# Kernel optimization log

Measured on AMD Instinct MI355X. Metric: run time of the kernel, lower is better.

The kernel has to match this reference:

```python
import jax, jax.numpy as jnp
import numpy as np

N, M, D, O = 16384, 4096, 256, 256

def setup_inputs() -> dict:
    key = jax.random.key(0)
    k1, k2, k3, k4, k5, k6, k7 = jax.random.split(key, 7)
    H_fine = jax.random.normal(k1, (N, D), dtype=jnp.float32)
    H_coarse = jax.random.normal(k2, (M, D), dtype=jnp.float32)
    inter_channel_adj = jax.random.randint(k3, (N, M), 0, 2).astype(jnp.float32)
    # attention = nn.Linear(2D, 1): weight vector [2D], bias scalar
    wa = jax.random.normal(k4, (2 * D,), dtype=jnp.float32) * (1.0 / np.sqrt(2 * D))
    ba = jax.random.normal(k5, (1,), dtype=jnp.float32) * 0.01
    # transform = nn.Linear(D, O), xavier_uniform weight
    lim = np.sqrt(6.0 / (D + O)).astype(np.float32)
    Wt = jax.random.uniform(k6, (O, D), minval=-lim, maxval=lim, dtype=jnp.float32)
    bt = jax.random.normal(k7, (O,), dtype=jnp.float32) * 0.01
    return {"H_fine": H_fine, "H_coarse": H_coarse,
            "inter_channel_adj": inter_channel_adj,
            "wa": wa, "ba": ba, "Wt": Wt, "bt": bt}

def reference(H_fine, H_coarse, inter_channel_adj, wa, ba, Wt, bt):
    d = H_fine.shape[-1]
    # additive attention: score_ij = [hf_i ; hc_j] . wa + b
    # = hf_i . wa[:d] + hc_j . wa[d:] + b  (avoids [N,M,2D] concat)
    sf = H_fine @ wa[:d]            # [N]
    sc = H_coarse @ wa[d:]          # [M]
    scores = sf[:, None] + sc[None, :] + ba[0]        # [N, M]
    masked = scores * inter_channel_adj               # [N, M]
    weights = jax.nn.softmax(masked, axis=-1)         # [N, M]
    attn_out = weights @ H_coarse                     # [N, D]
    attn_out = attn_out + H_fine                      # add_self=True
    out = attn_out @ Wt.T + bt                        # [N, O]
    return jax.nn.relu(out)
```

## Files before the change

### kernel.cpp

```cpp
#include <hip/hip_runtime.h>
#include <hip/hip_fp16.h>
#include <stdint.h>

#define N_ 16384
#define M_ 4096
#define D_ 256
#define O_ 256

#define WS_T    0
#define WS_U    65536
#define WS_R    81920
#define WS_WTP  98304
#define WS_BP   229376

typedef float  f32x4  __attribute__((ext_vector_type(4)));
typedef _Float16 half8 __attribute__((ext_vector_type(8)));

__device__ __forceinline__ unsigned short f2h(float f) {
  __half h = __float2half(f);
  unsigned short u;
  __builtin_memcpy(&u, &h, 2);
  return u;
}
__device__ __forceinline__ uint32_t hpack(float a, float b) {
  __half2 h = __floats2half2_rn(a, b);
  uint32_t u;
  __builtin_memcpy(&u, &h, 4);
  return u;
}

__global__ __launch_bounds__(256) void prep_kernel(
    const float* __restrict__ Hf, const float* __restrict__ Hc,
    const float* __restrict__ wa, const float* __restrict__ ba,
    const float* __restrict__ Wt, float* __restrict__ tv,
    float* __restrict__ uv, unsigned short* __restrict__ BP,
    unsigned short* __restrict__ WtP, float* __restrict__ Rv) {
  __shared__ float tile[64][65];
  __shared__ float red[4][64];
  int b = blockIdx.x;
  int t = threadIdx.x;
  if (b < 5120) {
    int wv = t >> 6, lane = t & 63;
    const float* X; const float* w; const float* bias; float* outv; int row;
    if (b < 4096) { X = Hf; w = wa;      bias = ba;      outv = tv; row = b * 4 + wv; }
    else          { X = Hc; w = wa + D_; bias = nullptr; outv = uv; row = (b - 4096) * 4 + wv; }
    const float4* x4 = (const float4*)(X + (size_t)row * D_);
    const float4* w4 = (const float4*)w;
    float4 xa = x4[lane], wa4 = w4[lane];
    float s = xa.x * wa4.x + xa.y * wa4.y + xa.z * wa4.z + xa.w * wa4.w;
#pragma unroll
    for (int off = 32; off > 0; off >>= 1) s += __shfl_xor(s, off);
    if (lane == 0) outv[row] = expf(s + (bias ? bias[0] : 0.0f));
  } else if (b < 5376) {
    int bb = b - 5120;
    int bk = bb >> 2;
    int bc = bb & 3;
    int k0 = bk * 64, col0 = bc * 64;
    int lane = t & 63, wv = t >> 6;
    int m = lane & 15, q = lane >> 4;
    float colsum = 0.0f;
#pragma unroll
    for (int i = 0; i < 16; ++i) {
      int e = t + 256 * i;
      int kk = e >> 6, cc = e & 63;
      float v = Hc[(size_t)(k0 + kk) * D_ + col0 + cc];
      tile[kk][cc] = v;
      colsum += v;
    }
    red[wv][t & 63] = colsum;
    __syncthreads();
    if (t < 64)
      atomicAdd(&Rv[col0 + t], red[0][t] + red[1][t] + red[2][t] + red[3][t]);
#pragma unroll
    for (int t8 = 0; t8 < 2; ++t8) {
      int tile_id = t8 * 4 + wv;
      int sub = tile_id >> 2, g = tile_id & 3;
      int kgg = bk * 2 + sub;
      int cgg = bc * 4 + g;
      unsigned short v8[8];
#pragma unroll
      for (int j = 0; j < 8; ++j)
        v8[j] = f2h(tile[sub * 32 + q * 8 + j][g * 16 + m]);
      *(uint4*)(BP + ((size_t)(kgg * 16 + cgg) * 64 + lane) * 8) = *(uint4*)v8;
    }
  } else {
    int tt = (b - 5376) * 256 + t;
    int lane = tt & 63, cg = (tt >> 6) & 15, kg = tt >> 10;
    int m = lane & 15, q = lane >> 4;
    const float* src = Wt + (size_t)(cg * 16 + m) * D_ + kg * 32 + q * 8;
    float4 w0 = *(const float4*)src, w1 = *(const float4*)(src + 4);
    unsigned short v8[8];
    v8[0] = f2h(w0.x); v8[1] = f2h(w0.y); v8[2] = f2h(w0.z); v8[3] = f2h(w0.w);
    v8[4] = f2h(w1.x); v8[5] = f2h(w1.y); v8[6] = f2h(w1.z); v8[7] = f2h(w1.w);
    *(uint4*)(WtP + (size_t)tt * 8) = *(uint4*)v8;
  }
}

__device__ __forceinline__ half8 buildA(half8 a, __half2 th,
                                        const __half2* up, __half2 mone) {
  uint32_t ai[4], ro[4];
  __builtin_memcpy(ai, &a, 16);
#pragma unroll
  for (int k = 0; k < 4; ++k) {
    __half2 w2 = __hfma2(th, up[k], mone);
    __half2 av;
    __builtin_memcpy(&av, &ai[k], 4);
    __half2 r = __hmul2(av, w2);
    __builtin_memcpy(&ro[k], &r, 4);
  }
  half8 res;
  __builtin_memcpy(&res, ro, 16);
  return res;
}

#define LOADS(KB)                                                             \
  _Pragma("unroll")                                                           \
  for (int p = 0; p < 4; ++p)                                                 \
    na[p] = *(const float4*)(arow + (KB) + p * 64 + t15 * 4);

#define TAIL(BUF, KB)                                                         \
  _Pragma("unroll")                                                           \
  for (int p = 0; p < 4; ++p) {                                               \
    int col = (KB) + p * 64 + t15 * 4;                                        \
    float4 u4 = *(const float4*)&u_lds[col];                                  \
    su = fmaf(na[p].x, u4.x, su); su = fmaf(na[p].y, u4.y, su);               \
    su = fmaf(na[p].z, u4.z, su); su = fmaf(na[p].w, u4.w, su);               \
    sc += (na[p].x + na[p].y) + (na[p].z + na[p].w);                          \
    uint2 hv;                                                                 \
    hv.x = hpack(na[p].x, na[p].y);                                           \
    hv.y = hpack(na[p].z, na[p].w);                                           \
    *(uint2*)&A_lds[BUF][srow][p * 64 + t15 * 4] = hv;                        \
  }

#define COMPUTE(C, BUF)                                                       \
  _Pragma("unroll")                                                           \
  for (int kgl = 0; kgl < 8; ++kgl) {                                         \
    int kg = (C) * 8 + kgl;                                                   \
    const unsigned short* bp = BP + ((size_t)(kg * 16 + w * 2)) * 512 + (size_t)lane * 8; \
    half8 bf0 = *(const half8*)(bp);                                          \
    half8 bf1 = *(const half8*)(bp + 512);                                    \
    uint4 uu = *(const uint4*)&u_h2[kg * 16 + q * 4];                         \
    __half2 up[4];                                                            \
    __builtin_memcpy(up, &uu, 16);                                            \
    half8 a0 = *(const half8*)&A_lds[BUF][m][kgl * 32 + q * 8];               \
    half8 a1 = *(const half8*)&A_lds[BUF][16 + m][kgl * 32 + q * 8];          \
    half8 af0 = buildA(a0, th0, up, mone);                                    \
    half8 af1 = buildA(a1, th1, up, mone);                                    \
    acc[0][0] = __builtin_amdgcn_mfma_f32_16x16x32_f16(af0, bf0, acc[0][0], 0, 0, 0); \
    acc[0][1] = __builtin_amdgcn_mfma_f32_16x16x32_f16(af0, bf1, acc[0][1], 0, 0, 0); \
    acc[1][0] = __builtin_amdgcn_mfma_f32_16x16x32_f16(af1, bf0, acc[1][0], 0, 0, 0); \
    acc[1][1] = __builtin_amdgcn_mfma_f32_16x16x32_f16(af1, bf1, acc[1][1], 0, 0, 0); \
  }

__global__ __launch_bounds__(512, 4) void mega_kernel(
    const float* __restrict__ adj, const unsigned short* __restrict__ BP,
    const float* __restrict__ tv, const float* __restrict__ uv,
    const float* __restrict__ Rv, const float* __restrict__ Hf,
    const unsigned short* __restrict__ WtP, const float* __restrict__ bt,
    float* __restrict__ out) {
  __shared__ __align__(16) char smem[59520];
  unsigned short (*A_lds)[32][272] = (unsigned short (*)[32][272])(smem);
  float* u_lds = (float*)(smem + 34816);
  uint32_t* u_h2 = (uint32_t*)(smem + 51200);
  float* Lsum_lds = (float*)(smem + 59392);
  unsigned short (*attn)[264] = (unsigned short (*)[264])(smem);

  int tid = threadIdx.x;
  int w = tid >> 6, lane = tid & 63;
  int q = lane >> 4, m = lane & 15;
  int srow = tid >> 4, t15 = tid & 15;
  int i0 = blockIdx.x * 32;

  const float* arow = adj + ((size_t)i0 + srow) * M_;
  float su = 0.f, sc = 0.f;
  float4 na[4];

  LOADS(0)

  for (int i = tid; i < M_ / 2; i += 512) {
    float2 u2 = *(const float2*)(uv + 2 * i);
    u_lds[2 * i] = u2.x; u_lds[2 * i + 1] = u2.y;
    u_h2[i] = hpack(u2.x, u2.y);
  }

  __half2 th0 = __float2half2_rn(tv[i0 + m]);
  __half2 th1 = __float2half2_rn(tv[i0 + 16 + m]);
  const __half2 mone = __float2half2_rn(-1.0f);

  f32x4 acc[2][2];
#pragma unroll
  for (int s = 0; s < 2; ++s)
#pragma unroll
    for (int n = 0; n < 2; ++n) acc[s][n] = (f32x4){0.f, 0.f, 0.f, 0.f};

  __syncthreads();
  TAIL(0, 0)
  __syncthreads();

#pragma unroll 1
  for (int c = 0; c < 16; ++c) {
    if (c < 15) { LOADS((c + 1) * 256) }
    COMPUTE(c, c & 1)
    if (c < 15) { TAIL((c + 1) & 1, (c + 1) * 256) }
    __syncthreads();
  }

#pragma unroll
  for (int off = 1; off < 16; off <<= 1) {
    su += __shfl_xor(su, off);
    sc += __shfl_xor(sc, off);
  }
  if (t15 == 0)
    Lsum_lds[srow] = tv[i0 + srow] * su - sc;
  __syncthreads();

  {
    float rv0 = Rv[w * 32 + m];
    float rv1 = Rv[w * 32 + 16 + m];
#pragma unroll
    for (int rt = 0; rt < 2; ++rt)
#pragma unroll
      for (int r = 0; r < 4; ++r) {
        int row = rt * 16 + q * 4 + r;
        float invL = 1.0f / (Lsum_lds[row] + (float)M_);
        size_t grow = (size_t)i0 + row;
        float h0 = Hf[grow * D_ + w * 32 + m];
        float h1 = Hf[grow * D_ + w * 32 + 16 + m];
        attn[row][w * 32 + m]      = f2h(fmaf(acc[rt][0][r] + rv0, invL, h0));
        attn[row][w * 32 + 16 + m] = f2h(fmaf(acc[rt][1][r] + rv1, invL, h1));
      }
  }
  __syncthreads();

  {
    int rt2 = w & 1, cq = w >> 1;
    f32x4 facc[4];
#pragma unroll
    for (int n = 0; n < 4; ++n) facc[n] = (f32x4){0.f, 0.f, 0.f, 0.f};
    const unsigned short* wwave = WtP + (size_t)(cq * 4) * 512 + (size_t)lane * 8;
#pragma unroll
    for (int kf = 0; kf < 8; ++kf) {
      half8 af = *(const half8*)&attn[rt2 * 16 + m][kf * 32 + q * 8];
#pragma unroll
      for (int n = 0; n < 4; ++n) {
        half8 bf = *(const half8*)(wwave + ((size_t)kf * 16 + n) * 512);
        facc[n] = __builtin_amdgcn_mfma_f32_16x16x32_f16(af, bf, facc[n], 0, 0, 0);
      }
    }
#pragma unroll
    for (int n = 0; n < 4; ++n) {
      int col = cq * 64 + n * 16 + m;
      float b = bt[col];
#pragma unroll
      for (int r = 0; r < 4; ++r) {
        size_t row = (size_t)i0 + rt2 * 16 + q * 4 + r;
        out[row * O_ + col] = fmaxf(facc[n][r] + b, 0.0f);
      }
    }
  }
}

extern "C" void kernel_launch(void* const* d_in, const int* in_sizes, int n_in,
                              void* d_out, int out_size, void* d_ws, size_t ws_size,
                              hipStream_t stream) {
  const float* Hf  = (const float*)d_in[0];
  const float* Hc  = (const float*)d_in[1];
  const float* adj = (const float*)d_in[2];
  const float* wa  = (const float*)d_in[3];
  const float* ba  = (const float*)d_in[4];
  const float* Wt  = (const float*)d_in[5];
  const float* bt  = (const float*)d_in[6];
  float* out = (float*)d_out;

  char* ws = (char*)d_ws;
  float* tv   = (float*)(ws + WS_T);
  float* uv   = (float*)(ws + WS_U);
  float* Rv   = (float*)(ws + WS_R);
  unsigned short* WtP = (unsigned short*)(ws + WS_WTP);
  unsigned short* BP  = (unsigned short*)(ws + WS_BP);

  hipMemsetAsync(Rv, 0, D_ * sizeof(float), stream);

  prep_kernel<<<5408, 256, 0, stream>>>(Hf, Hc, wa, ba, Wt, tv, uv, BP, WtP, Rv);
  mega_kernel<<<512, 512, 0, stream>>>(adj, BP, tv, uv, Rv, Hf, WtP, bt, out);
}
```

Measured before the change: 440.9 us.

## Encode adjacency as ballot bitmasks and stage B fragments through LDS

The adjacency tile is no longer converted to fp16 and stored in LDS. Each wave now reads rows with coalesced per-lane loads and compresses them into bitmasks with __ballot, and the MFMA A fragments are built by masking the precomputed t*u-1 values with those bits. The packed B operand is now staged cooperatively into LDS per 128-column chunk instead of each wave reading it from global memory. The chunk loop is restructured with register double buffering. The bitmask path assumes the adjacency holds only 0/1 values, and the loop adds more barriers per chunk and a larger LDS footprint, which may reduce occupancy.

```diff
diff --git a/kernel.cpp b/kernel.cpp
--- a/kernel.cpp
+++ b/kernel.cpp
@@ -96,56 +96,87 @@
   }
 }
 
-__device__ __forceinline__ half8 buildA(half8 a, __half2 th,
-                                        const __half2* up, __half2 mone) {
-  uint32_t ai[4], ro[4];
-  __builtin_memcpy(ai, &a, 16);
-#pragma unroll
-  for (int k = 0; k < 4; ++k) {
-    __half2 w2 = __hfma2(th, up[k], mone);
-    __half2 av;
-    __builtin_memcpy(&av, &ai[k], 4);
-    __half2 r = __hmul2(av, w2);
-    __builtin_memcpy(&ro[k], &r, 4);
-  }
-  half8 res;
-  __builtin_memcpy(&res, ro, 16);
-  return res;
-}
-
-#define LOADS(KB)                                                             \
+__device__ __forceinline__ half8 frag_f16(uint32_t bits, __half2 th,
+                                          const __half2* up, __half2 mone) {
+  union { half8 h; uint32_t u[4]; } r;
+#pragma unroll
+  for (int p = 0; p < 4; ++p) {
+    __half2 v = __hfma2(th, up[p], mone);
+    uint32_t c;
+    __builtin_memcpy(&c, &v, 4);
+    uint32_t mlo = (uint32_t)((int32_t)(bits << (31 - 2 * p)) >> 31);
+    uint32_t mhi = (uint32_t)((int32_t)(bits << (30 - 2 * p)) >> 31);
+    r.u[p] = c & ((mlo & 0x0000FFFFu) | (mhi & 0xFFFF0000u));
+  }
+  return r.h;
+}
+
+#define STAGE(C)                                                              \
+  {                                                                           \
+    const uint4* gsrc = (const uint4*)BP + (size_t)(C) * 4096 + tid;          \
+    uint4 q0 = gsrc[0],        q1 = gsrc[512],      q2 = gsrc[1024];          \
+    uint4 q3 = gsrc[1536],     q4 = gsrc[2048],     q5 = gsrc[2560];          \
+    uint4 q6 = gsrc[3072],     q7 = gsrc[3584];                               \
+    uint4* ld = (uint4*)B_lds + tid;                                          \
+    ld[0] = q0;    ld[512] = q1;  ld[1024] = q2; ld[1536] = q3;               \
+    ld[2048] = q4; ld[2560] = q5; ld[3072] = q6; ld[3584] = q7;               \
+  }
+
+#define LOADS(n0, n1, n2, n3, KB)                                             \
   _Pragma("unroll")                                                           \
-  for (int p = 0; p < 4; ++p)                                                 \
-    na[p] = *(const float4*)(arow + (KB) + p * 64 + t15 * 4);
-
-#define TAIL(BUF, KB)                                                         \
+  for (int cc = 0; cc < 2; ++cc) {                                            \
+    n0[cc] = ar[(size_t)0 * M_ + (KB) + cc * 64 + lane];                      \
+    n1[cc] = ar[(size_t)1 * M_ + (KB) + cc * 64 + lane];                      \
+    n2[cc] = ar[(size_t)2 * M_ + (KB) + cc * 64 + lane];                      \
+    n3[cc] = ar[(size_t)3 * M_ + (KB) + cc * 64 + lane];                      \
+  }
+
+#define TAIL(n0, n1, n2, n3, KB)                                              \
+  {                                                                           \
+    unsigned long long bal0[2], bal1[2], bal2[2], bal3[2];                    \
+    _Pragma("unroll")                                                         \
+    for (int cc = 0; cc < 2; ++cc) {                                          \
+      float uvv = uv[(KB) + cc * 64 + lane];                                  \
+      bal0[cc] = __ballot(n0[cc] != 0.0f);                                    \
+      bal1[cc] = __ballot(n1[cc] != 0.0f);                                    \
+      bal2[cc] = __ballot(n2[cc] != 0.0f);                                    \
+      bal3[cc] = __ballot(n3[cc] != 0.0f);                                    \
+      su[0] = fmaf(n0[cc], uvv, su[0]);                                       \
+      su[1] = fmaf(n1[cc], uvv, su[1]);                                       \
+      su[2] = fmaf(n2[cc], uvv, su[2]);                                       \
+      su[3] = fmaf(n3[cc], uvv, su[3]);                                       \
+    }                                                                         \
+    sc[0] += n0[0] + n0[1];                                                   \
+    sc[1] += n1[0] + n1[1];                                                   \
+    sc[2] += n2[0] + n2[1];                                                   \
+    sc[3] += n3[0] + n3[1];                                                   \
+    if (lane < 16) {                                                          \
+      int rowsel = lane >> 2, ccs = (lane >> 1) & 1, hi = lane & 1;           \
+      unsigned long long v0 = ccs ? bal0[1] : bal0[0];                        \
+      unsigned long long v1 = ccs ? bal1[1] : bal1[0];                        \
+      unsigned long long v2 = ccs ? bal2[1] : bal2[0];                        \
+      unsigned long long v3 = ccs ? bal3[1] : bal3[0];                        \
+      unsigned long long v = rowsel == 0 ? v0 : rowsel == 1 ? v1              \
+                           : rowsel == 2 ? v2 : v3;                           \
+      bits_lds[w * 4 + rowsel][lane & 3] =                                    \
+          hi ? (unsigned int)(v >> 32) : (unsigned int)v;                     \
+    }                                                                         \
+  }
+
+#define COMPUTE(C)                                                            \
   _Pragma("unroll")                                                           \
-  for (int p = 0; p < 4; ++p) {                                               \
-    int col = (KB) + p * 64 + t15 * 4;                                        \
-    float4 u4 = *(const float4*)&u_lds[col];                                  \
-    su = fmaf(na[p].x, u4.x, su); su = fmaf(na[p].y, u4.y, su);               \
-    su = fmaf(na[p].z, u4.z, su); su = fmaf(na[p].w, u4.w, su);               \
-    sc += (na[p].x + na[p].y) + (na[p].z + na[p].w);                          \
-    uint2 hv;                                                                 \
-    hv.x = hpack(na[p].x, na[p].y);                                           \
-    hv.y = hpack(na[p].z, na[p].w);                                           \
-    *(uint2*)&A_lds[BUF][srow][p * 64 + t15 * 4] = hv;                        \
-  }
-
-#define COMPUTE(C, BUF)                                                       \
-  _Pragma("unroll")                                                           \
-  for (int kgl = 0; kgl < 8; ++kgl) {                                         \
-    int kg = (C) * 8 + kgl;                                                   \
-    const unsigned short* bp = BP + ((size_t)(kg * 16 + w * 2)) * 512 + (size_t)lane * 8; \
+  for (int kgc = 0; kgc < 4; ++kgc) {                                         \
+    int kg = (C) * 4 + kgc;                                                   \
+    uint32_t b0 = bits_lds[m][kgc];                                           \
+    uint32_t b1 = bits_lds[16 + m][kgc];                                      \
+    uint4 uu = *(const uint4*)&u_h2[kg * 16 + q * 4];                         \
+    const unsigned short* bp = B_lds + ((size_t)(kgc * 16 + w * 2) * 64 + lane) * 8; \
     half8 bf0 = *(const half8*)(bp);                                          \
     half8 bf1 = *(const half8*)(bp + 512);                                    \
-    uint4 uu = *(const uint4*)&u_h2[kg * 16 + q * 4];                         \
     __half2 up[4];                                                            \
     __builtin_memcpy(up, &uu, 16);                                            \
-    half8 a0 = *(const half8*)&A_lds[BUF][m][kgl * 32 + q * 8];               \
-    half8 a1 = *(const half8*)&A_lds[BUF][16 + m][kgl * 32 + q * 8];          \
-    half8 af0 = buildA(a0, th0, up, mone);                                    \
-    half8 af1 = buildA(a1, th1, up, mone);                                    \
+    half8 af0 = frag_f16((b0 >> sh) & 0xffu, th0, up, mone);                  \
+    half8 af1 = frag_f16((b1 >> sh) & 0xffu, th1, up, mone);                  \
     acc[0][0] = __builtin_amdgcn_mfma_f32_16x16x32_f16(af0, bf0, acc[0][0], 0, 0, 0); \
     acc[0][1] = __builtin_amdgcn_mfma_f32_16x16x32_f16(af0, bf1, acc[0][1], 0, 0, 0); \
     acc[1][0] = __builtin_amdgcn_mfma_f32_16x16x32_f16(af1, bf0, acc[1][0], 0, 0, 0); \
@@ -158,28 +189,27 @@
     const float* __restrict__ Rv, const float* __restrict__ Hf,
     const unsigned short* __restrict__ WtP, const float* __restrict__ bt,
     float* __restrict__ out) {
-  __shared__ __align__(16) char smem[59520];
-  unsigned short (*A_lds)[32][272] = (unsigned short (*)[32][272])(smem);
-  float* u_lds = (float*)(smem + 34816);
-  uint32_t* u_h2 = (uint32_t*)(smem + 51200);
-  float* Lsum_lds = (float*)(smem + 59392);
+  __shared__ __align__(16) char smem[74496];
+  unsigned short* B_lds = (unsigned short*)(smem);
+  uint32_t* u_h2 = (uint32_t*)(smem + 65536);
+  unsigned int (*bits_lds)[5] = (unsigned int (*)[5])(smem + 73728);
+  float* Lsum_lds = (float*)(smem + 74368);
   unsigned short (*attn)[264] = (unsigned short (*)[264])(smem);
 
   int tid = threadIdx.x;
   int w = tid >> 6, lane = tid & 63;
   int q = lane >> 4, m = lane & 15;
-  int srow = tid >> 4, t15 = tid & 15;
+  int sh = q * 8;
   int i0 = blockIdx.x * 32;
 
-  const float* arow = adj + ((size_t)i0 + srow) * M_;
-  float su = 0.f, sc = 0.f;
-  float4 na[4];
-
-  LOADS(0)
-
+  const float* ar = adj + ((size_t)i0 + w * 4) * M_;
+  float su[4] = {0.f, 0.f, 0.f, 0.f}, sc[4] = {0.f, 0.f, 0.f, 0.f};
+  float sA0[2], sA1[2], sA2[2], sA3[2];
+  float sB0[2], sB1[2], sB2[2], sB3[2];
+
+  LOADS(sA0, sA1, sA2, sA3, 0)
   for (int i = tid; i < M_ / 2; i += 512) {
     float2 u2 = *(const float2*)(uv + 2 * i);
-    u_lds[2 * i] = u2.x; u_lds[2 * i + 1] = u2.y;
     u_h2[i] = hpack(u2.x, u2.y);
   }
 
@@ -193,25 +223,36 @@
 #pragma unroll
     for (int n = 0; n < 2; ++n) acc[s][n] = (f32x4){0.f, 0.f, 0.f, 0.f};
 
-  __syncthreads();
-  TAIL(0, 0)
-  __syncthreads();
-
 #pragma unroll 1
-  for (int c = 0; c < 16; ++c) {
-    if (c < 15) { LOADS((c + 1) * 256) }
-    COMPUTE(c, c & 1)
-    if (c < 15) { TAIL((c + 1) & 1, (c + 1) * 256) }
-    __syncthreads();
-  }
-
-#pragma unroll
-  for (int off = 1; off < 16; off <<= 1) {
-    su += __shfl_xor(su, off);
-    sc += __shfl_xor(sc, off);
-  }
-  if (t15 == 0)
-    Lsum_lds[srow] = tv[i0 + srow] * su - sc;
+  for (int cc2 = 0; cc2 < 16; ++cc2) {
+    int c0 = cc2 * 2;
+    STAGE(c0)
+    LOADS(sB0, sB1, sB2, sB3, (c0 + 1) * 128)
+    TAIL(sA0, sA1, sA2, sA3, c0 * 128)
+    __syncthreads();
+    COMPUTE(c0)
+    __syncthreads();
+    int c1 = c0 + 1;
+    STAGE(c1)
+    if (c1 + 1 < 32) { LOADS(sA0, sA1, sA2, sA3, (c1 + 1) * 128) }
+    TAIL(sB0, sB1, sB2, sB3, c1 * 128)
+    __syncthreads();
+    COMPUTE(c1)
+    __syncthreads();
+  }
+
+#pragma unroll
+  for (int off = 32; off > 0; off >>= 1) {
+    su[0] += __shfl_xor(su[0], off); sc[0] += __shfl_xor(sc[0], off);
+    su[1] += __shfl_xor(su[1], off); sc[1] += __shfl_xor(sc[1], off);
+    su[2] += __shfl_xor(su[2], off); sc[2] += __shfl_xor(sc[2], off);
+    su[3] += __shfl_xor(su[3], off); sc[3] += __shfl_xor(sc[3], off);
+  }
+  if (lane == 0) {
+#pragma unroll
+    for (int j = 0; j < 4; ++j)
+      Lsum_lds[w * 4 + j] = tv[i0 + w * 4 + j] * su[j] - sc[j];
+  }
   __syncthreads();
 
   {
@@ -222,8 +263,8 @@
 #pragma unroll
       for (int r = 0; r < 4; ++r) {
         int row = rt * 16 + q * 4 + r;
+        size_t grow = (size_t)i0 + row;
         float invL = 1.0f / (Lsum_lds[row] + (float)M_);
-        size_t grow = (size_t)i0 + row;
         float h0 = Hf[grow * D_ + w * 32 + m];
         float h1 = Hf[grow * D_ + w * 32 + 16 + m];
         attn[row][w * 32 + m]      = f2h(fmaf(acc[rt][0][r] + rv0, invL, h0));
```

New measurement: 430.3 us, median of 2. 2.4% less time.
